# Kernel tuning notes

Measured on AMD Instinct MI355X. Metric: run time of the kernel, lower is better.

Reference implementation:

```python
import jax, jax.numpy as jnp
import numpy as np

B, S, H, NH = 2, 2048, 1024, 16
HD = H // NH
SCALE = float(H) ** 0.5  # note: source scales by sqrt(hidden_dim), not sqrt(head_dim)
EPS = 1e-5


def setup_inputs() -> dict:
    key = jax.random.key(0)
    ks = jax.random.split(key, 16)
    s = 0.02
    return {
        "q": jax.random.normal(ks[0], (B, S, H), jnp.float32),
        "k": jax.random.normal(ks[1], (B, S, H), jnp.float32),
        "v": jax.random.normal(ks[2], (B, S, H), jnp.float32),
        "mask": jax.random.randint(ks[3], (B, 1, S, S), 0, 2, jnp.int32),
        "Wq": jax.random.normal(ks[4], (H, H), jnp.float32) * s,
        "bq": jnp.zeros((H,), jnp.float32),
        "Wk": jax.random.normal(ks[5], (H, H), jnp.float32) * s,
        "bk": jnp.zeros((H,), jnp.float32),
        "Wv": jax.random.normal(ks[6], (H, H), jnp.float32) * s,
        "bv": jnp.zeros((H,), jnp.float32),
        "Wfc": jax.random.normal(ks[7], (H, H), jnp.float32) * s,
        "bfc": jnp.zeros((H,), jnp.float32),
        "gamma": jnp.ones((H,), jnp.float32),
        "beta": jnp.zeros((H,), jnp.float32),
    }


def reference(q, k, v, mask, Wq, bq, Wk, bk, Wv, bv, Wfc, bfc, gamma, beta):
    residual = q
    qh = (q @ Wq + bq).reshape(B, S, NH, HD)
    kh = (k @ Wk + bk).reshape(B, S, NH, HD)
    vh = (v @ Wv + bv).reshape(B, S, NH, HD)
    # full [B, NH, S, S] score matrix, as in the source
    energy = jnp.einsum('nqhd,nkhd->nhqk', qh, kh)
    energy = jnp.where(mask == 0, jnp.float32(-1e9), energy)
    attn = jax.nn.softmax(energy / SCALE, axis=3)  # dropout p=0.0 -> identity
    out = jnp.einsum('nhqk,nkhd->nqhd', attn, vh).reshape(B, S, H)
    y = out @ Wfc + bfc + residual
    mu = jnp.mean(y, axis=-1, keepdims=True)
    var = jnp.mean((y - mu) ** 2, axis=-1, keepdims=True)
    return gamma * (y - mu) / jnp.sqrt(var + EPS) + beta
```

## Files before the change

kernel.cpp:

```cpp
#include <hip/hip_runtime.h>
#include <hip/hip_bf16.h>

#define S_LEN  2048
#define HDIM   1024
#define NHEADS 16
#define HEADD  64
#define BATCH  2
#define MTOT   (BATCH * S_LEN)
#define K2EXP  0.04508422f

typedef __attribute__((ext_vector_type(8)))  __bf16 bf16x8;
typedef __attribute__((ext_vector_type(4)))  __bf16 bf16x4;
typedef __attribute__((ext_vector_type(4)))  float  f32x4;
typedef __attribute__((ext_vector_type(16))) float  f32x16;

__device__ __forceinline__ void gload16(const void* g, void* l) {
  __builtin_amdgcn_global_load_lds(
      (const __attribute__((address_space(1))) void*)g,
      (__attribute__((address_space(3))) void*)l, 16, 0, 0);
}
__device__ __forceinline__ bf16x8 lds_rd(const __bf16* base, int row, int bcol) {
  const char* p = (const char*)base + row * 128 + (bcol ^ ((row & 7) << 4));
  return *(const bf16x8*)p;
}
__device__ __forceinline__ unsigned cvtpk_bf16(float lo, float hi) {
  unsigned r;
  asm("v_cvt_pk_bf16_f32 %0, %1, %2" : "=v"(r) : "v"(lo), "v"(hi));
  return r;
}
__device__ __forceinline__ void plswap(unsigned& a, unsigned& b) {
  asm volatile("v_permlane32_swap_b32 %0, %1" : "+v"(a), "+v"(b));
}

__global__ __launch_bounds__(256)
void cvt_kernel(const float* __restrict__ q, const float* __restrict__ k,
                const float* __restrict__ v, __bf16* __restrict__ Qc,
                __bf16* __restrict__ Kc, __bf16* __restrict__ Vc)
{
  const int z = blockIdx.z;
  const float* src = (z == 0) ? q : (z == 1) ? k : v;
  __bf16* dst = (z == 0) ? Qc : (z == 1) ? Kc : Vc;
  const size_t i = ((size_t)blockIdx.x * 256 + threadIdx.x) * 8;
  const float4 a = *(const float4*)&src[i];
  const float4 c = *(const float4*)&src[i + 4];
  bf16x8 o;
  o[0] = (__bf16)a.x; o[1] = (__bf16)a.y; o[2] = (__bf16)a.z; o[3] = (__bf16)a.w;
  o[4] = (__bf16)c.x; o[5] = (__bf16)c.y; o[6] = (__bf16)c.z; o[7] = (__bf16)c.w;
  *(bf16x8*)&dst[i] = o;
}

__global__ __launch_bounds__(256)
void maskpack_kernel(const int* __restrict__ mask, unsigned* __restrict__ mbT)
{
  const size_t idx = (size_t)blockIdx.x * 256 + threadIdx.x;
  const int m = mask[idx];
  const unsigned long long bal = __ballot(m != 0);
  if ((threadIdx.x & 63) == 0) {
    const int b   = (int)(idx >> 22);
    const int qq  = (int)(idx >> 11) & 2047;
    const int kvw = ((int)idx & 2047) >> 5;
    mbT[((size_t)b * 64 + kvw) * S_LEN + qq]       = (unsigned)bal;
    mbT[((size_t)b * 64 + kvw + 1) * S_LEN + qq]   = (unsigned)(bal >> 32);
  }
}

__global__ __launch_bounds__(256)
void transw_kernel(const float* __restrict__ Wq, const float* __restrict__ Wk,
                   const float* __restrict__ Wv, const float* __restrict__ Wfc,
                   __bf16* __restrict__ Wt)
{
  __shared__ float T[64][65];
  const int z = blockIdx.z;
  const float* W = (z == 0) ? Wq : (z == 1) ? Wk : (z == 2) ? Wv : Wfc;
  __bf16* O = Wt + (size_t)z * HDIM * HDIM;
  const int k0 = blockIdx.x * 64, n0 = blockIdx.y * 64;
  const int tid = threadIdx.x;
  const int r  = tid >> 4;
  const int c4 = (tid & 15) * 4;
  #pragma unroll
  for (int p = 0; p < 4; ++p) {
    const int row = r + p * 16;
    const float4 vv = *(const float4*)&W[(size_t)(k0 + row) * HDIM + n0 + c4];
    T[row][c4 + 0] = vv.x; T[row][c4 + 1] = vv.y;
    T[row][c4 + 2] = vv.z; T[row][c4 + 3] = vv.w;
  }
  __syncthreads();
  #pragma unroll
  for (int p = 0; p < 4; ++p) {
    const int n = r + p * 16;
    bf16x4 o;
    #pragma unroll
    for (int i = 0; i < 4; ++i) o[i] = (__bf16)T[c4 + i][n];
    *(bf16x4*)&O[(size_t)(n0 + n) * HDIM + k0 + c4] = o;
  }
}

__global__ __launch_bounds__(256)
void vtrans_kernel(const __bf16* __restrict__ Vb, __bf16* __restrict__ Vtg)
{
  __shared__ __bf16 T[64][72];
  const int b = blockIdx.z, h = blockIdx.y, kv0 = blockIdx.x * 64;
  const int tid = threadIdx.x;
  {
    const int kv = tid >> 2, c16 = (tid & 3) * 16;
    const __bf16* src = &Vb[((size_t)b * S_LEN + kv0 + kv) * HDIM + h * HEADD + c16];
    *(bf16x8*)&T[kv][c16]     = *(const bf16x8*)src;
    *(bf16x8*)&T[kv][c16 + 8] = *(const bf16x8*)(src + 8);
  }
  __syncthreads();
  {
    const int hd = tid >> 2, kv16 = (tid & 3) * 16;
    bf16x8 o0, o1;
    #pragma unroll
    for (int i = 0; i < 8; ++i) { o0[i] = T[kv16 + i][hd]; o1[i] = T[kv16 + 8 + i][hd]; }
    __bf16* dst = &Vtg[((size_t)(b * NHEADS + h) * HEADD + hd) * S_LEN + kv0 + kv16];
    *(bf16x8*)dst = o0; *(bf16x8*)(dst + 8) = o1;
  }
}

template<int MODE>
__device__ __forceinline__ void gemm_body(
    const __bf16* __restrict__ A, const __bf16* __restrict__ Wt,
    const float* __restrict__ bias, const float* __restrict__ resid,
    __bf16* __restrict__ Ob, float* __restrict__ Of)
{
  __shared__ __bf16 As[2][128][64];
  __shared__ __bf16 Bs[2][128][64];
  const int tid = threadIdx.x, lane = tid & 63, w = tid >> 6;
  const int fr = lane & 15, k8 = (lane >> 4) * 8;
  const int wr = w >> 1, wc = w & 1;
  const int m0 = blockIdx.y * 128, n0 = blockIdx.x * 128;
  const int srow8 = lane >> 3, slot = lane & 7;

  f32x4 acc[4][4] = {};

  #define G_STAGE(kt, bf)                                                    \
    {                                                                        \
      _Pragma("unroll")                                                      \
      for (int c = 0; c < 4; ++c) {                                          \
        const int ra = w * 32 + c * 8 + srow8;                               \
        gload16(&A[(size_t)(m0 + ra) * HDIM + (kt) * 64 + ((slot ^ (ra & 7)) * 8)], \
                (void*)&As[bf][w * 32 + c * 8][0]);                          \
      }                                                                      \
      _Pragma("unroll")                                                      \
      for (int c = 0; c < 4; ++c) {                                          \
        const int rb = w * 32 + c * 8 + srow8;                               \
        gload16(&Wt[(size_t)(n0 + rb) * HDIM + (kt) * 64 + ((slot ^ (rb & 7)) * 8)], \
                (void*)&Bs[bf][w * 32 + c * 8][0]);                          \
      }                                                                      \
    }

  #define G_COMPUTE(bf)                                                      \
    {                                                                        \
      _Pragma("unroll")                                                      \
      for (int kk = 0; kk < 64; kk += 32) {                                  \
        bf16x8 a[4], b[4];                                                   \
        _Pragma("unroll")                                                    \
        for (int i = 0; i < 4; ++i)                                          \
          a[i] = lds_rd(&As[bf][0][0], wr * 64 + i * 16 + fr, (kk + k8) * 2);\
        _Pragma("unroll")                                                    \
        for (int j = 0; j < 4; ++j)                                          \
          b[j] = lds_rd(&Bs[bf][0][0], wc * 64 + j * 16 + fr, (kk + k8) * 2);\
        _Pragma("unroll")                                                    \
        for (int i = 0; i < 4; ++i)                                          \
          _Pragma("unroll")                                                  \
          for (int j = 0; j < 4; ++j)                                        \
            acc[i][j] = __builtin_amdgcn_mfma_f32_16x16x32_bf16(a[i], b[j], acc[i][j], 0, 0, 0); \
      }                                                                      \
    }

  G_STAGE(0, 0)
  for (int kt = 0; kt < 15; ++kt) {
    G_STAGE(kt + 1, (kt + 1) & 1)
    asm volatile("s_waitcnt vmcnt(8)" ::: "memory");
    __builtin_amdgcn_s_barrier();
    __builtin_amdgcn_sched_barrier(0);
    G_COMPUTE(kt & 1)
    __builtin_amdgcn_sched_barrier(0);
    __builtin_amdgcn_s_barrier();
  }
  asm volatile("s_waitcnt vmcnt(0)" ::: "memory");
  __builtin_amdgcn_s_barrier();
  G_COMPUTE(1)

  const int rg = (lane >> 4) * 4;
  #pragma unroll
  for (int i = 0; i < 4; ++i) {
    #pragma unroll
    for (int j = 0; j < 4; ++j) {
      #pragma unroll
      for (int r = 0; r < 4; ++r) {
        const int row = m0 + wr * 64 + i * 16 + rg + r;
        const int col = n0 + wc * 64 + j * 16 + fr;
        const float vv = acc[i][j][r] + bias[col];
        if constexpr (MODE == 0) {
          Ob[(size_t)row * HDIM + col] = (__bf16)vv;
        } else {
          Of[(size_t)row * HDIM + col] = vv + resid[(size_t)row * HDIM + col];
        }
      }
    }
  }
  #undef G_STAGE
  #undef G_COMPUTE
}

__global__ __launch_bounds__(256)
void qkv_kernel(const __bf16* __restrict__ Qc, const __bf16* __restrict__ Kc,
                const __bf16* __restrict__ Vc, const __bf16* __restrict__ Wt,
                const float* __restrict__ bq, const float* __restrict__ bk,
                const float* __restrict__ bv,
                __bf16* __restrict__ Qb, __bf16* __restrict__ Kb,
                __bf16* __restrict__ Vb)
{
  const int z = blockIdx.z;
  const __bf16* A  = (z == 0) ? Qc : (z == 1) ? Kc : Vc;
  const float* bb  = (z == 0) ? bq : (z == 1) ? bk : bv;
  __bf16*      O   = (z == 0) ? Qb : (z == 1) ? Kb : Vb;
  gemm_body<0>(A, Wt + (size_t)z * HDIM * HDIM, bb, nullptr, O, nullptr);
}

__global__ __launch_bounds__(256)
void fc_kernel(const __bf16* __restrict__ A, const __bf16* __restrict__ Wt,
               const float* __restrict__ bias, const float* __restrict__ resid,
               float* __restrict__ Of)
{
  gemm_body<1>(A, Wt + (size_t)3 * HDIM * HDIM, bias, resid, nullptr, Of);
}

__global__ __launch_bounds__(512)
void attn_kernel(const __bf16* __restrict__ Qb, const __bf16* __restrict__ Kb,
                 const __bf16* __restrict__ Vtg, const unsigned* __restrict__ mbT,
                 __bf16* __restrict__ AO)
{
  __shared__ __bf16 Ks[2][64][64];
  __shared__ __bf16 Vt[2][64][64];
  __shared__ __align__(16) float Lsm[8][32];

  const int bh = blockIdx.x, b = bh >> 4, h = bh & 15;
  const int tid = threadIdx.x, lane = tid & 63, w = tid >> 6;
  const int fr = lane & 31, hi = lane >> 5;
  const int qw = blockIdx.y * 256 + w * 32;
  const int q  = qw + fr;

  bf16x8 qf[4];
  #pragma unroll
  for (int st = 0; st < 4; ++st)
    qf[st] = *(const bf16x8*)&Qb[((size_t)b * S_LEN + q) * HDIM + h * HEADD + st * 16 + hi * 8];

  const int srow = w * 8 + (lane >> 3), slot = lane & 7;
  const __bf16* ksrc = Kb  + ((size_t)b * S_LEN + srow) * HDIM + h * HEADD + (slot ^ (srow & 7)) * 8;
  const __bf16* vsrc = Vtg + ((size_t)bh * HEADD + srow) * S_LEN + (slot ^ (srow & 7)) * 8;
  const unsigned* mrow = mbT + (size_t)b * 64 * S_LEN + q;

  f32x16 o0 = {}, o1 = {};
  float lsum = 0.f;
  unsigned mv0, mv1, nv0 = 0, nv1 = 0;

  mv0 = mrow[0];
  mv1 = mrow[S_LEN];
  gload16(ksrc, (void*)&Ks[0][w * 8][0]);
  gload16(vsrc, (void*)&Vt[0][w * 8][0]);

  for (int t = 0; t < 32; ++t) {
    const int buf = t & 1;
    if (t < 31) {
      nv0 = mrow[(size_t)(2 * t + 2) * S_LEN];
      nv1 = mrow[(size_t)(2 * t + 3) * S_LEN];
      gload16(ksrc + (size_t)(t + 1) * 64 * HDIM, (void*)&Ks[buf ^ 1][w * 8][0]);
      gload16(vsrc + (t + 1) * 64,                (void*)&Vt[buf ^ 1][w * 8][0]);
      asm volatile("s_waitcnt vmcnt(4)" ::: "memory");
    } else {
      asm volatile("s_waitcnt vmcnt(0)" ::: "memory");
    }
    __builtin_amdgcn_s_barrier();
    __builtin_amdgcn_sched_barrier(0);

    f32x16 s0 = {}, s1 = {};
    #pragma unroll
    for (int st = 0; st < 4; ++st) {
      const bf16x8 ka0 = lds_rd(&Ks[buf][0][0], fr,      st * 32 + hi * 16);
      const bf16x8 ka1 = lds_rd(&Ks[buf][0][0], 32 + fr, st * 32 + hi * 16);
      s0 = __builtin_amdgcn_mfma_f32_32x32x16_bf16(ka0, qf[st], s0, 0, 0, 0);
      s1 = __builtin_amdgcn_mfma_f32_32x32x16_bf16(ka1, qf[st], s1, 0, 0, 0);
    }

    float pp[32];
    const int kb = 4 * hi;
    #pragma unroll
    for (int j = 0; j < 16; ++j) {
      const int kvl = (j & 3) + 8 * (j >> 2) + kb;
      const float e0 = __builtin_amdgcn_exp2f(s0[j] * K2EXP);
      const float e1 = __builtin_amdgcn_exp2f(s1[j] * K2EXP);
      pp[j]      = ((mv0 >> kvl) & 1u) ? e0 : 0.f;
      pp[16 + j] = ((mv1 >> kvl) & 1u) ? e1 : 0.f;
      lsum += pp[j] + pp[16 + j];
    }

    bf16x8 pa[4];
    #pragma unroll
    for (int g = 0; g < 4; ++g) {
      const int o = (g >> 1) * 16 + (g & 1) * 8;
      unsigned x  = cvtpk_bf16(pp[o + 0], pp[o + 1]);
      unsigned x2 = cvtpk_bf16(pp[o + 2], pp[o + 3]);
      unsigned y  = cvtpk_bf16(pp[o + 4], pp[o + 5]);
      unsigned y2 = cvtpk_bf16(pp[o + 6], pp[o + 7]);
      plswap(x, y);
      plswap(x2, y2);
      union { unsigned u[4]; bf16x8 v; } uu;
      uu.u[0] = x; uu.u[1] = x2; uu.u[2] = y; uu.u[3] = y2;
      pa[g] = uu.v;
    }

    #pragma unroll
    for (int g = 0; g < 4; ++g) {
      const bf16x8 vb0 = lds_rd(&Vt[buf][0][0], fr,      g * 32 + hi * 16);
      const bf16x8 vb1 = lds_rd(&Vt[buf][0][0], 32 + fr, g * 32 + hi * 16);
      o0 = __builtin_amdgcn_mfma_f32_32x32x16_bf16(pa[g], vb0, o0, 0, 0, 0);
      o1 = __builtin_amdgcn_mfma_f32_32x32x16_bf16(pa[g], vb1, o1, 0, 0, 0);
    }

    mv0 = nv0; mv1 = nv1;
    __builtin_amdgcn_sched_barrier(0);
    __builtin_amdgcn_s_barrier();
  }

  const float lt = lsum + __shfl_xor(lsum, 32);
  if (hi == 0) Lsm[w][fr] = lt;
  #pragma unroll
  for (int g = 0; g < 4; ++g) {
    const f32x4 L = *(const f32x4*)&Lsm[w][g * 8 + hi * 4];
    #pragma unroll
    for (int r = 0; r < 4; ++r) {
      const float inv = __builtin_amdgcn_rcpf(L[r]);
      const int j = g * 4 + r;
      const int qq = qw + g * 8 + hi * 4 + r;
      AO[((size_t)b * S_LEN + qq) * HDIM + h * HEADD + fr]      = (__bf16)(o0[j] * inv);
      AO[((size_t)b * S_LEN + qq) * HDIM + h * HEADD + 32 + fr] = (__bf16)(o1[j] * inv);
    }
  }
}

__global__ __launch_bounds__(256)
void ln_kernel(float* __restrict__ y, const float* __restrict__ gamma,
               const float* __restrict__ beta)
{
  __shared__ float red[8];
  const int tid = threadIdx.x;
  float* p = y + (size_t)blockIdx.x * HDIM;

  float4 vv = *(const float4*)&p[tid * 4];
  float s  = vv.x + vv.y + vv.z + vv.w;
  float ss = vv.x * vv.x + vv.y * vv.y + vv.z * vv.z + vv.w * vv.w;
  #pragma unroll
  for (int d = 1; d < 64; d <<= 1) {
    s  += __shfl_xor(s, d);
    ss += __shfl_xor(ss, d);
  }
  const int wid = tid >> 6;
  if ((tid & 63) == 0) { red[wid * 2] = s; red[wid * 2 + 1] = ss; }
  __syncthreads();
  s  = red[0] + red[2] + red[4] + red[6];
  ss = red[1] + red[3] + red[5] + red[7];
  const float mean = s * (1.0f / HDIM);
  const float var  = ss * (1.0f / HDIM) - mean * mean;
  const float inv  = rsqrtf(var + 1e-5f);

  const float4 g  = *(const float4*)&gamma[tid * 4];
  const float4 bt = *(const float4*)&beta[tid * 4];
  vv.x = (vv.x - mean) * inv * g.x + bt.x;
  vv.y = (vv.y - mean) * inv * g.y + bt.y;
  vv.z = (vv.z - mean) * inv * g.z + bt.z;
  vv.w = (vv.w - mean) * inv * g.w + bt.w;
  *(float4*)&p[tid * 4] = vv;
}

extern "C" void kernel_launch(void* const* d_in, const int* in_sizes, int n_in,
                              void* d_out, int out_size, void* d_ws, size_t ws_size,
                              hipStream_t stream) {
  const float* q     = (const float*)d_in[0];
  const float* k     = (const float*)d_in[1];
  const float* v     = (const float*)d_in[2];
  const int*   mask  = (const int*)  d_in[3];
  const float* Wq    = (const float*)d_in[4];
  const float* bq    = (const float*)d_in[5];
  const float* Wk    = (const float*)d_in[6];
  const float* bk    = (const float*)d_in[7];
  const float* Wv    = (const float*)d_in[8];
  const float* bv    = (const float*)d_in[9];
  const float* Wfc   = (const float*)d_in[10];
  const float* bfc   = (const float*)d_in[11];
  const float* gamma = (const float*)d_in[12];
  const float* beta  = (const float*)d_in[13];
  float* out = (float*)d_out;

  char* ws = (char*)d_ws;
  const size_t MB16 = (size_t)MTOT * HDIM * 2;
  unsigned* mbT = (unsigned*)ws;
  __bf16* Wt  = (__bf16*)(ws + (1u << 20));
  __bf16* Qc  = (__bf16*)(ws + (1u << 20) + 4 * (size_t)HDIM * HDIM * 2);
  __bf16* Kc  = (__bf16*)((char*)Qc + MB16);
  __bf16* Vc  = (__bf16*)((char*)Kc + MB16);
  __bf16* Qb  = (__bf16*)((char*)Vc + MB16);
  __bf16* Kb  = (__bf16*)((char*)Qb + MB16);
  __bf16* Vb  = (__bf16*)((char*)Kb + MB16);
  __bf16* Vtg = Qc;
  __bf16* AO  = Kc;

  const dim3 blk(256);

  cvt_kernel<<<dim3(MTOT * HDIM / 8 / 256, 1, 3), blk, 0, stream>>>(q, k, v, Qc, Kc, Vc);
  maskpack_kernel<<<dim3((size_t)BATCH * S_LEN * S_LEN / 256), blk, 0, stream>>>(mask, mbT);
  transw_kernel<<<dim3(16, 16, 4), blk, 0, stream>>>(Wq, Wk, Wv, Wfc, Wt);

  qkv_kernel<<<dim3(HDIM / 128, MTOT / 128, 3), blk, 0, stream>>>(
      Qc, Kc, Vc, Wt, bq, bk, bv, Qb, Kb, Vb);

  vtrans_kernel<<<dim3(S_LEN / 64, NHEADS, BATCH), blk, 0, stream>>>(Vb, Vtg);

  attn_kernel<<<dim3(BATCH * NHEADS, S_LEN / 256), dim3(512), 0, stream>>>(
      Qb, Kb, Vtg, mbT, AO);

  fc_kernel<<<dim3(HDIM / 128, MTOT / 128), blk, 0, stream>>>(
      AO, Wt, bfc, q, out);

  ln_kernel<<<dim3(MTOT), blk, 0, stream>>>(out, gamma, beta);
}
```

Before: 169.9 us.

## Fold softmax scale into Wq, fuse V transpose into projection, retile attention

The softmax exp2 scale is folded into the transposed Wq weights and the Q bias, so the attention inner loop no longer multiplies scores. The V projection now writes its output directly in the per-head transposed layout, which removes the separate vtrans kernel and its extra memory round trip. GEMM blocks are remapped in an XCD-aware swizzle, s_setprio is raised around MFMA sections, and attention moves from 512-thread blocks to 256-thread blocks with more blocks in the grid. Rounding the scaled Wq to bf16 slightly changes numerics, and the transposed V stores are narrow 8-byte scattered writes.

```diff
diff --git a/kernel.cpp b/kernel.cpp
--- a/kernel.cpp
+++ b/kernel.cpp
@@ -72,6 +72,7 @@
   __shared__ float T[64][65];
   const int z = blockIdx.z;
   const float* W = (z == 0) ? Wq : (z == 1) ? Wk : (z == 2) ? Wv : Wfc;
+  const float sc = (z == 0) ? K2EXP : 1.0f;
   __bf16* O = Wt + (size_t)z * HDIM * HDIM;
   const int k0 = blockIdx.x * 64, n0 = blockIdx.y * 64;
   const int tid = threadIdx.x;
@@ -90,46 +91,27 @@
     const int n = r + p * 16;
     bf16x4 o;
     #pragma unroll
-    for (int i = 0; i < 4; ++i) o[i] = (__bf16)T[c4 + i][n];
+    for (int i = 0; i < 4; ++i) o[i] = (__bf16)(T[c4 + i][n] * sc);
     *(bf16x4*)&O[(size_t)(n0 + n) * HDIM + k0 + c4] = o;
-  }
-}
-
-__global__ __launch_bounds__(256)
-void vtrans_kernel(const __bf16* __restrict__ Vb, __bf16* __restrict__ Vtg)
-{
-  __shared__ __bf16 T[64][72];
-  const int b = blockIdx.z, h = blockIdx.y, kv0 = blockIdx.x * 64;
-  const int tid = threadIdx.x;
-  {
-    const int kv = tid >> 2, c16 = (tid & 3) * 16;
-    const __bf16* src = &Vb[((size_t)b * S_LEN + kv0 + kv) * HDIM + h * HEADD + c16];
-    *(bf16x8*)&T[kv][c16]     = *(const bf16x8*)src;
-    *(bf16x8*)&T[kv][c16 + 8] = *(const bf16x8*)(src + 8);
-  }
-  __syncthreads();
-  {
-    const int hd = tid >> 2, kv16 = (tid & 3) * 16;
-    bf16x8 o0, o1;
-    #pragma unroll
-    for (int i = 0; i < 8; ++i) { o0[i] = T[kv16 + i][hd]; o1[i] = T[kv16 + 8 + i][hd]; }
-    __bf16* dst = &Vtg[((size_t)(b * NHEADS + h) * HEADD + hd) * S_LEN + kv0 + kv16];
-    *(bf16x8*)dst = o0; *(bf16x8*)(dst + 8) = o1;
   }
 }
 
 template<int MODE>
 __device__ __forceinline__ void gemm_body(
     const __bf16* __restrict__ A, const __bf16* __restrict__ Wt,
-    const float* __restrict__ bias, const float* __restrict__ resid,
-    __bf16* __restrict__ Ob, float* __restrict__ Of)
+    const float* __restrict__ bias, float bscale,
+    const float* __restrict__ resid,
+    __bf16* __restrict__ Ob, float* __restrict__ Of, __bf16* __restrict__ Vtg)
 {
   __shared__ __bf16 As[2][128][64];
   __shared__ __bf16 Bs[2][128][64];
   const int tid = threadIdx.x, lane = tid & 63, w = tid >> 6;
   const int fr = lane & 15, k8 = (lane >> 4) * 8;
   const int wr = w >> 1, wc = w & 1;
-  const int m0 = blockIdx.y * 128, n0 = blockIdx.x * 128;
+  const int f   = blockIdx.x + gridDim.x * blockIdx.y;
+  const int cpx = (gridDim.x * gridDim.y) >> 3;
+  const int fs  = (f & 7) * cpx + (f >> 3);
+  const int m0 = (fs / gridDim.x) * 128, n0 = (fs % gridDim.x) * 128;
   const int srow8 = lane >> 3, slot = lane & 7;
 
   f32x4 acc[4][4] = {};
@@ -175,7 +157,9 @@
     asm volatile("s_waitcnt vmcnt(8)" ::: "memory");
     __builtin_amdgcn_s_barrier();
     __builtin_amdgcn_sched_barrier(0);
+    __builtin_amdgcn_s_setprio(1);
     G_COMPUTE(kt & 1)
+    __builtin_amdgcn_s_setprio(0);
     __builtin_amdgcn_sched_barrier(0);
     __builtin_amdgcn_s_barrier();
   }
@@ -188,15 +172,25 @@
   for (int i = 0; i < 4; ++i) {
     #pragma unroll
     for (int j = 0; j < 4; ++j) {
-      #pragma unroll
-      for (int r = 0; r < 4; ++r) {
-        const int row = m0 + wr * 64 + i * 16 + rg + r;
-        const int col = n0 + wc * 64 + j * 16 + fr;
-        const float vv = acc[i][j][r] + bias[col];
-        if constexpr (MODE == 0) {
-          Ob[(size_t)row * HDIM + col] = (__bf16)vv;
-        } else {
-          Of[(size_t)row * HDIM + col] = vv + resid[(size_t)row * HDIM + col];
+      const int col = n0 + wc * 64 + j * 16 + fr;
+      if constexpr (MODE == 2) {
+        const int h = col >> 6, hd = col & 63;
+        const int row = m0 + wr * 64 + i * 16 + rg;
+        const int bq = row >> 11, qq = row & 2047;
+        bf16x4 o;
+        #pragma unroll
+        for (int r = 0; r < 4; ++r) o[r] = (__bf16)(acc[i][j][r] + bias[col]);
+        *(bf16x4*)&Vtg[(((size_t)bq * NHEADS + h) * HEADD + hd) * S_LEN + qq] = o;
+      } else {
+        #pragma unroll
+        for (int r = 0; r < 4; ++r) {
+          const int row = m0 + wr * 64 + i * 16 + rg + r;
+          if constexpr (MODE == 0) {
+            Ob[(size_t)row * HDIM + col] = (__bf16)(acc[i][j][r] + bias[col] * bscale);
+          } else {
+            Of[(size_t)row * HDIM + col] =
+                acc[i][j][r] + bias[col] + resid[(size_t)row * HDIM + col];
+          }
         }
       }
     }
@@ -206,18 +200,22 @@
 }
 
 __global__ __launch_bounds__(256)
-void qkv_kernel(const __bf16* __restrict__ Qc, const __bf16* __restrict__ Kc,
-                const __bf16* __restrict__ Vc, const __bf16* __restrict__ Wt,
-                const float* __restrict__ bq, const float* __restrict__ bk,
-                const float* __restrict__ bv,
-                __bf16* __restrict__ Qb, __bf16* __restrict__ Kb,
-                __bf16* __restrict__ Vb)
+void qk_kernel(const __bf16* __restrict__ Qc, const __bf16* __restrict__ Kc,
+               const __bf16* __restrict__ Wt,
+               const float* __restrict__ bq, const float* __restrict__ bk,
+               __bf16* __restrict__ Qb, __bf16* __restrict__ Kb)
 {
   const int z = blockIdx.z;
-  const __bf16* A  = (z == 0) ? Qc : (z == 1) ? Kc : Vc;
-  const float* bb  = (z == 0) ? bq : (z == 1) ? bk : bv;
-  __bf16*      O   = (z == 0) ? Qb : (z == 1) ? Kb : Vb;
-  gemm_body<0>(A, Wt + (size_t)z * HDIM * HDIM, bb, nullptr, O, nullptr);
+  gemm_body<0>(z ? Kc : Qc, Wt + (size_t)z * HDIM * HDIM, z ? bk : bq,
+               z ? 1.0f : K2EXP, nullptr, z ? Kb : Qb, nullptr, nullptr);
+}
+
+__global__ __launch_bounds__(256)
+void vproj_kernel(const __bf16* __restrict__ Vc, const __bf16* __restrict__ Wt,
+                  const float* __restrict__ bv, __bf16* __restrict__ Vtg)
+{
+  gemm_body<2>(Vc, Wt + (size_t)2 * HDIM * HDIM, bv, 1.0f, nullptr,
+               nullptr, nullptr, Vtg);
 }
 
 __global__ __launch_bounds__(256)
@@ -225,22 +223,23 @@
                const float* __restrict__ bias, const float* __restrict__ resid,
                float* __restrict__ Of)
 {
-  gemm_body<1>(A, Wt + (size_t)3 * HDIM * HDIM, bias, resid, nullptr, Of);
-}
-
-__global__ __launch_bounds__(512)
+  gemm_body<1>(A, Wt + (size_t)3 * HDIM * HDIM, bias, 1.0f, resid,
+               nullptr, Of, nullptr);
+}
+
+__global__ __launch_bounds__(256)
 void attn_kernel(const __bf16* __restrict__ Qb, const __bf16* __restrict__ Kb,
                  const __bf16* __restrict__ Vtg, const unsigned* __restrict__ mbT,
                  __bf16* __restrict__ AO)
 {
   __shared__ __bf16 Ks[2][64][64];
   __shared__ __bf16 Vt[2][64][64];
-  __shared__ __align__(16) float Lsm[8][32];
+  __shared__ __align__(16) float Lsm[4][32];
 
   const int bh = blockIdx.x, b = bh >> 4, h = bh & 15;
   const int tid = threadIdx.x, lane = tid & 63, w = tid >> 6;
   const int fr = lane & 31, hi = lane >> 5;
-  const int qw = blockIdx.y * 256 + w * 32;
+  const int qw = blockIdx.y * 128 + w * 32;
   const int q  = qw + fr;
 
   bf16x8 qf[4];
@@ -248,7 +247,7 @@
   for (int st = 0; st < 4; ++st)
     qf[st] = *(const bf16x8*)&Qb[((size_t)b * S_LEN + q) * HDIM + h * HEADD + st * 16 + hi * 8];
 
-  const int srow = w * 8 + (lane >> 3), slot = lane & 7;
+  const int srow = w * 16 + (lane >> 3), slot = lane & 7;
   const __bf16* ksrc = Kb  + ((size_t)b * S_LEN + srow) * HDIM + h * HEADD + (slot ^ (srow & 7)) * 8;
   const __bf16* vsrc = Vtg + ((size_t)bh * HEADD + srow) * S_LEN + (slot ^ (srow & 7)) * 8;
   const unsigned* mrow = mbT + (size_t)b * 64 * S_LEN + q;
@@ -259,17 +258,23 @@
 
   mv0 = mrow[0];
   mv1 = mrow[S_LEN];
-  gload16(ksrc, (void*)&Ks[0][w * 8][0]);
-  gload16(vsrc, (void*)&Vt[0][w * 8][0]);
+  gload16(ksrc,            (void*)&Ks[0][w * 16][0]);
+  gload16(ksrc + 8 * HDIM, (void*)&Ks[0][w * 16 + 8][0]);
+  gload16(vsrc,             (void*)&Vt[0][w * 16][0]);
+  gload16(vsrc + 8 * S_LEN, (void*)&Vt[0][w * 16 + 8][0]);
 
   for (int t = 0; t < 32; ++t) {
     const int buf = t & 1;
     if (t < 31) {
       nv0 = mrow[(size_t)(2 * t + 2) * S_LEN];
       nv1 = mrow[(size_t)(2 * t + 3) * S_LEN];
-      gload16(ksrc + (size_t)(t + 1) * 64 * HDIM, (void*)&Ks[buf ^ 1][w * 8][0]);
-      gload16(vsrc + (t + 1) * 64,                (void*)&Vt[buf ^ 1][w * 8][0]);
-      asm volatile("s_waitcnt vmcnt(4)" ::: "memory");
+      const __bf16* kp = ksrc + (size_t)(t + 1) * 64 * HDIM;
+      const __bf16* vp = vsrc + (t + 1) * 64;
+      gload16(kp,            (void*)&Ks[buf ^ 1][w * 16][0]);
+      gload16(kp + 8 * HDIM, (void*)&Ks[buf ^ 1][w * 16 + 8][0]);
+      gload16(vp,             (void*)&Vt[buf ^ 1][w * 16][0]);
+      gload16(vp + 8 * S_LEN, (void*)&Vt[buf ^ 1][w * 16 + 8][0]);
+      asm volatile("s_waitcnt vmcnt(6)" ::: "memory");
     } else {
       asm volatile("s_waitcnt vmcnt(0)" ::: "memory");
     }
@@ -277,6 +282,7 @@
     __builtin_amdgcn_sched_barrier(0);
 
     f32x16 s0 = {}, s1 = {};
+    __builtin_amdgcn_s_setprio(1);
     #pragma unroll
     for (int st = 0; st < 4; ++st) {
       const bf16x8 ka0 = lds_rd(&Ks[buf][0][0], fr,      st * 32 + hi * 16);
@@ -284,14 +290,15 @@
       s0 = __builtin_amdgcn_mfma_f32_32x32x16_bf16(ka0, qf[st], s0, 0, 0, 0);
       s1 = __builtin_amdgcn_mfma_f32_32x32x16_bf16(ka1, qf[st], s1, 0, 0, 0);
     }
+    __builtin_amdgcn_s_setprio(0);
 
     float pp[32];
     const int kb = 4 * hi;
     #pragma unroll
     for (int j = 0; j < 16; ++j) {
       const int kvl = (j & 3) + 8 * (j >> 2) + kb;
-      const float e0 = __builtin_amdgcn_exp2f(s0[j] * K2EXP);
-      const float e1 = __builtin_amdgcn_exp2f(s1[j] * K2EXP);
+      const float e0 = __builtin_amdgcn_exp2f(s0[j]);
+      const float e1 = __builtin_amdgcn_exp2f(s1[j]);
       pp[j]      = ((mv0 >> kvl) & 1u) ? e0 : 0.f;
       pp[16 + j] = ((mv1 >> kvl) & 1u) ? e1 : 0.f;
       lsum += pp[j] + pp[16 + j];
@@ -312,6 +319,7 @@
       pa[g] = uu.v;
     }
 
+    __builtin_amdgcn_s_setprio(1);
     #pragma unroll
     for (int g = 0; g < 4; ++g) {
       const bf16x8 vb0 = lds_rd(&Vt[buf][0][0], fr,      g * 32 + hi * 16);
@@ -319,6 +327,7 @@
       o0 = __builtin_amdgcn_mfma_f32_32x32x16_bf16(pa[g], vb0, o0, 0, 0, 0);
       o1 = __builtin_amdgcn_mfma_f32_32x32x16_bf16(pa[g], vb1, o1, 0, 0, 0);
     }
+    __builtin_amdgcn_s_setprio(0);
 
     mv0 = nv0; mv1 = nv1;
     __builtin_amdgcn_sched_barrier(0);
@@ -403,8 +412,7 @@
   __bf16* Vc  = (__bf16*)((char*)Kc + MB16);
   __bf16* Qb  = (__bf16*)((char*)Vc + MB16);
   __bf16* Kb  = (__bf16*)((char*)Qb + MB16);
-  __bf16* Vb  = (__bf16*)((char*)Kb + MB16);
-  __bf16* Vtg = Qc;
+  __bf16* Vtg = (__bf16*)((char*)Kb + MB16);
   __bf16* AO  = Kc;
 
   const dim3 blk(256);
@@ -413,12 +421,12 @@
   maskpack_kernel<<<dim3((size_t)BATCH * S_LEN * S_LEN / 256), blk, 0, stream>>>(mask, mbT);
   transw_kernel<<<dim3(16, 16, 4), blk, 0, stream>>>(Wq, Wk, Wv, Wfc, Wt);
 
-  qkv_kernel<<<dim3(HDIM / 128, MTOT / 128, 3), blk, 0, stream>>>(
-      Qc, Kc, Vc, Wt, bq, bk, bv, Qb, Kb, Vb);
-
-  vtrans_kernel<<<dim3(S_LEN / 64, NHEADS, BATCH), blk, 0, stream>>>(Vb, Vtg);
-
-  attn_kernel<<<dim3(BATCH * NHEADS, S_LEN / 256), dim3(512), 0, stream>>>(
+  qk_kernel<<<dim3(HDIM / 128, MTOT / 128, 2), blk, 0, stream>>>(
+      Qc, Kc, Wt, bq, bk, Qb, Kb);
+  vproj_kernel<<<dim3(HDIM / 128, MTOT / 128), blk, 0, stream>>>(
+      Vc, Wt, bv, Vtg);
+
+  attn_kernel<<<dim3(BATCH * NHEADS, S_LEN / 128), blk, 0, stream>>>(
       Qb, Kb, Vtg, mbT, AO);
 
   fc_kernel<<<dim3(HDIM / 128, MTOT / 128), blk, 0, stream>>>(
```

Result: no change. 170.2 us (+0.1%).
